# Optimization experiments

Hardware: AMD Instinct MI355X
Metric: run time of the kernel (lower is better)

The kernel has to match this reference:

```python
import jax, jax.numpy as jnp
import numpy as np

D = 1024
H = 16
HD = D // H
MLP = 4 * D
EPS = 1e-5


def layernorm(x, g, b):
    mu = jnp.mean(x, axis=-1, keepdims=True)
    var = jnp.mean(jnp.square(x - mu), axis=-1, keepdims=True)
    return (x - mu) * jax.lax.rsqrt(var + EPS) * g + b


def setup_inputs() -> dict:
    key = jax.random.key(0)
    ks = jax.random.split(key, 12)
    s = 0.02
    return {
        "x": jax.random.normal(ks[0], (2, 2048, D), jnp.float32),
        "ln1_g": jnp.ones((D,), jnp.float32),
        "ln1_b": jnp.zeros((D,), jnp.float32),
        "lnm_g": jnp.ones((D,), jnp.float32),
        "lnm_b": jnp.zeros((D,), jnp.float32),
        "qkv_w": jax.random.normal(ks[1], (D, 3 * D), jnp.float32) * s,
        "qkv_b": jnp.zeros((3 * D,), jnp.float32),
        "proj_w": jax.random.normal(ks[2], (D, D), jnp.float32) * s,
        "proj_b": jnp.zeros((D,), jnp.float32),
        "fc1_w": jax.random.normal(ks[3], (D, MLP), jnp.float32) * s,
        "fc1_b": jnp.zeros((MLP,), jnp.float32),
        "fc2_w": jax.random.normal(ks[4], (MLP, D), jnp.float32) * s,
        "fc2_b": jnp.zeros((D,), jnp.float32),
    }


def reference(x, ln1_g, ln1_b, lnm_g, lnm_b, qkv_w, qkv_b, proj_w, proj_b,
              fc1_w, fc1_b, fc2_w, fc2_b):
    B, N, _ = x.shape
    scale = HD ** -0.5
    # --- self-attention on norm1(x) ---
    h = layernorm(x, ln1_g, ln1_b)
    qkv = h @ qkv_w + qkv_b                       # [B, N, 3D]
    qkv = qkv.reshape(B, N, 3, H, HD)
    q, k, v = qkv[:, :, 0], qkv[:, :, 1], qkv[:, :, 2]  # [B, N, H, HD]
    attn = jnp.einsum("bqhd,bkhd->bhqk", q, k) * scale
    attn = jax.nn.softmax(attn, axis=-1)
    o = jnp.einsum("bhqk,bkhd->bqhd", attn, v).reshape(B, N, D)
    x = x + (o @ proj_w + proj_b)
    # --- MLP ---
    m = layernorm(x, lnm_g, lnm_b)
    m = jax.nn.gelu(m @ fc1_w + fc1_b, approximate=False)
    x = x + (m @ fc2_w + fc2_b)
    return x
```

## Files before the change

kernel.cpp:

```cpp
#include <hip/hip_runtime.h>

typedef __bf16 bf16_t;
typedef bf16_t bf16x8 __attribute__((ext_vector_type(8)));
typedef float f32x4 __attribute__((ext_vector_type(4)));
typedef unsigned short u16x8 __attribute__((ext_vector_type(8)));

#define MFMA(a, b, c) __builtin_amdgcn_mfma_f32_16x16x32_bf16(a, b, c, 0, 0, 0)

__device__ inline float exp2_fast(float x) {
  float r;
  asm volatile("v_exp_f32 %0, %1" : "=v"(r) : "v"(x));
  return r;
}

__device__ inline void gll16(const bf16_t* g, bf16_t* l) {
  __builtin_amdgcn_global_load_lds(
      (const __attribute__((address_space(1))) unsigned int*)(g),
      (__attribute__((address_space(3))) unsigned int*)(l), 16, 0, 0);
}

__device__ inline float gelu_f(float v) {
  float ax = fabsf(v) * 0.70710678118f;
  float t = __builtin_amdgcn_rcpf(1.0f + 0.3275911f * ax);
  float p = ((((1.061405429f * t - 1.453152027f) * t + 1.421413741f) * t -
              0.284496736f) * t + 0.254829592f) * t;
  float e = exp2_fast(-ax * ax * 1.4426950408889634f);
  float erf = 1.0f - p * e;
  erf = v < 0.f ? -erf : erf;
  return 0.5f * v * (1.0f + erf);
}

__global__ __launch_bounds__(256) void ln_kernel(const float* __restrict__ x,
                                                 const float* __restrict__ g,
                                                 const float* __restrict__ b,
                                                 bf16_t* __restrict__ out) {
  long row = blockIdx.x;
  const float4* xr = (const float4*)(x + row * 1024);
  float4 v = xr[threadIdx.x];
  float s = v.x + v.y + v.z + v.w;
  float s2 = v.x * v.x + v.y * v.y + v.z * v.z + v.w * v.w;
#pragma unroll
  for (int m = 32; m >= 1; m >>= 1) {
    s += __shfl_xor(s, m);
    s2 += __shfl_xor(s2, m);
  }
  __shared__ float red[8];
  int wid = threadIdx.x >> 6;
  if ((threadIdx.x & 63) == 0) {
    red[wid] = s;
    red[4 + wid] = s2;
  }
  __syncthreads();
  s = red[0] + red[1] + red[2] + red[3];
  s2 = red[4] + red[5] + red[6] + red[7];
  float mu = s * (1.f / 1024.f);
  float rs = rsqrtf(s2 * (1.f / 1024.f) - mu * mu + 1e-5f);
  float4 gv = ((const float4*)g)[threadIdx.x];
  float4 bv = ((const float4*)b)[threadIdx.x];
  bf16_t o0 = (bf16_t)((v.x - mu) * rs * gv.x + bv.x);
  bf16_t o1 = (bf16_t)((v.y - mu) * rs * gv.y + bv.y);
  bf16_t o2 = (bf16_t)((v.z - mu) * rs * gv.z + bv.z);
  bf16_t o3 = (bf16_t)((v.w - mu) * rs * gv.w + bv.w);
  ushort4 pk;
  pk.x = *(unsigned short*)&o0;
  pk.y = *(unsigned short*)&o1;
  pk.z = *(unsigned short*)&o2;
  pk.w = *(unsigned short*)&o3;
  *(ushort4*)(out + row * 1024 + threadIdx.x * 4) = pk;
}

__global__ void wconv_kernel(const float* __restrict__ W, bf16_t* __restrict__ Wt,
                             int K, int N) {
  __shared__ float t[32][33];
  int n0 = blockIdx.x * 32, k0 = blockIdx.y * 32;
#pragma unroll
  for (int s = 0; s < 4; s++) {
    int k = threadIdx.y + s * 8;
    t[k][threadIdx.x] = W[(long)(k0 + k) * N + n0 + threadIdx.x];
  }
  __syncthreads();
#pragma unroll
  for (int s = 0; s < 4; s++) {
    int n = threadIdx.y + s * 8;
    Wt[(long)(n0 + n) * K + k0 + threadIdx.x] = (bf16_t)t[threadIdx.x][n];
  }
}

#define STAGE_PTR(DA, DB, k0)                \
  gll16(ga + (k0), DA + w * 1024);           \
  gll16(ga + (k0) + rowstep, DA + w * 1024 + 512); \
  gll16(gb + (k0), DB + w * 1024);           \
  gll16(gb + (k0) + rowstep, DB + w * 1024 + 512);

#define COMPUTE(LA, LB)                                                \
  {                                                                    \
    bf16x8 af[4], bfr[4];                                              \
    _Pragma("unroll") for (int mt = 0; mt < 4; mt++) af[mt] =          \
        *(const bf16x8*)(LA + (wm + mt * 16 + l15) * 32 + quad * 8);   \
    _Pragma("unroll") for (int nt = 0; nt < 4; nt++) bfr[nt] =         \
        *(const bf16x8*)(LB + (wn + nt * 16 + l15) * 32 + quad * 8);   \
    _Pragma("unroll") for (int mt = 0; mt < 4; mt++)                   \
        _Pragma("unroll") for (int nt = 0; nt < 4; nt++) acc[mt][nt] = \
            MFMA(af[mt], bfr[nt], acc[mt][nt]);                        \
  }

#define WB4 asm volatile("s_waitcnt vmcnt(4)\ns_barrier" ::: "memory")
#define WB0 asm volatile("s_waitcnt vmcnt(0)\ns_barrier" ::: "memory")

__global__ __launch_bounds__(256) void gemm_kernel(
    const bf16_t* __restrict__ A, const bf16_t* __restrict__ Bt,
    const float* __restrict__ bias, const float* __restrict__ resid,
    void* __restrict__ Cout, int M, int N, int K, int epi) {
  __shared__ bf16_t lA0[128 * 32], lB0[128 * 32];
  __shared__ bf16_t lA1[128 * 32], lB1[128 * 32];
  __shared__ bf16_t lA2[128 * 32], lB2[128 * 32];
  int tid = threadIdx.x;
  int bn = blockIdx.x, bm = blockIdx.y;
  int kchunk = K / gridDim.z;
  int kbeg = blockIdx.z * kchunk, kend = kbeg + kchunk;

  int lane = tid & 63, w = tid >> 6;
  int quad = lane >> 4, l15 = lane & 15;
  int wm = (w & 1) * 64, wn = (w >> 1) * 64;

  f32x4 acc[4][4];
#pragma unroll
  for (int i = 0; i < 4; i++)
#pragma unroll
    for (int j = 0; j < 4; j++) acc[i][j] = (f32x4){0.f, 0.f, 0.f, 0.f};

  const bf16_t* ga = A + (long)(bm * 128 + w * 32 + (lane >> 2)) * K + (lane & 3) * 8;
  const bf16_t* gb = Bt + (long)(bn * 128 + w * 32 + (lane >> 2)) * K + (lane & 3) * 8;
  long rowstep = (long)16 * K;

  int nit = (kend - kbeg) >> 5;
  bf16_t *A0 = lA0, *A1 = lA1, *A2 = lA2;
  bf16_t *B0 = lB0, *B1 = lB1, *B2 = lB2;
  STAGE_PTR(A0, B0, kbeg);
  STAGE_PTR(A1, B1, kbeg + 32);
  for (int i = 0; i < nit; i++) {
    if (i + 1 < nit) { WB4; } else { WB0; }
    if (i + 2 < nit) {
      int ks = kbeg + (i + 2) * 32;
      STAGE_PTR(A2, B2, ks);
    }
    COMPUTE(A0, B0);
    bf16_t* t;
    t = A0; A0 = A1; A1 = A2; A2 = t;
    t = B0; B0 = B1; B1 = B2; B2 = t;
  }

#pragma unroll
  for (int mt = 0; mt < 4; mt++) {
#pragma unroll
    for (int r = 0; r < 4; r++) {
      long row = bm * 128 + wm + mt * 16 + quad * 4 + r;
#pragma unroll
      for (int nt = 0; nt < 4; nt++) {
        int col = bn * 128 + wn + nt * 16 + l15;
        long idx = row * N + col;
        if (epi == 3) {
          ((float*)Cout)[(long)blockIdx.z * M * N + idx] = acc[mt][nt][r];
        } else {
          float v = acc[mt][nt][r] + bias[col];
          if (epi == 1) {
            ((float*)Cout)[idx] = v + resid[idx];
          } else if (epi == 2) {
            ((bf16_t*)Cout)[idx] = (bf16_t)gelu_f(v);
          } else {
            ((bf16_t*)Cout)[idx] = (bf16_t)v;
          }
        }
      }
    }
  }
}

__global__ __launch_bounds__(256) void reduce2_kernel(const float* __restrict__ p0,
                                                      const float* __restrict__ p1,
                                                      const float* __restrict__ bias,
                                                      const float* __restrict__ resid,
                                                      float* __restrict__ out) {
  long i = (long)blockIdx.x * 256 + threadIdx.x;
  float4 a = ((const float4*)p0)[i];
  float4 c = ((const float4*)p1)[i];
  float4 r = ((const float4*)resid)[i];
  float4 bv = ((const float4*)bias)[i & 255];
  float4 o;
  o.x = a.x + c.x + r.x + bv.x;
  o.y = a.y + c.y + r.y + bv.y;
  o.z = a.z + c.z + r.z + bv.z;
  o.w = a.w + c.w + r.w + bv.w;
  ((float4*)out)[i] = o;
}

#define LDV 72

__global__ __launch_bounds__(256) void attn_kernel(const bf16_t* __restrict__ qkv,
                                                   bf16_t* __restrict__ o) {
  const int LD = 3072;
  int flat = blockIdx.x;
  int slot = flat >> 3;
  int bh = (flat & 7) * 4 + (slot >> 5);
  int qt = slot & 31;
  int h = bh & 15, b = bh >> 4;

  int tid = threadIdx.x, w = tid >> 6, lane = tid & 63;
  int quad = lane >> 4, l15 = lane & 15;
  int qrow = qt * 64 + w * 16;
  const bf16_t* base = qkv + (long)b * 2048 * LD + h * 64;
  const bf16_t* Qp = base;
  const bf16_t* Kp = base + 1024;
  const bf16_t* Vp = base + 2048;

  __shared__ bf16_t lK[64 * 64];
  __shared__ bf16_t lV[64 * LDV];
  __shared__ bf16_t lP[4][16 * LDV];
  bf16_t* myp = lP[w];

  const bf16_t* kg =
      Kp + (long)(w * 16 + (lane >> 3)) * LD + (((lane & 7) ^ (lane >> 3)) & 7) * 8;
  bf16_t* lkd = lK + w * 1024;
  int kk = tid & 31;
  int d0 = (tid >> 5) * 8;
  const bf16_t* vg = Vp + (long)(2 * kk) * LD + d0;
  unsigned int* lvw = (unsigned int*)lV;

  bf16x8 qf[2];
#pragma unroll
  for (int d = 0; d < 2; d++)
    qf[d] = *(const bf16x8*)(Qp + (long)(qrow + l15) * LD + d * 32 + quad * 8);

  f32x4 oacc[4];
#pragma unroll
  for (int t = 0; t < 4; t++) oacc[t] = (f32x4){0.f, 0.f, 0.f, 0.f};
  float li_p[4] = {0.f, 0.f, 0.f, 0.f};
  const float c2 = 0.18033688011112042f;

  int sw0 = (quad ^ l15) & 7;
  int sw1 = ((quad + 4) ^ l15) & 7;

  for (int kt = 0; kt < 2048; kt += 64) {
    long koff = (long)kt * LD;
    u16x8 va = *(const u16x8*)(vg + koff);
    u16x8 vb = *(const u16x8*)(vg + koff + LD);
    __syncthreads();
    gll16(kg + koff, lkd);
    gll16(kg + koff + 8 * (long)LD, lkd + 512);
#pragma unroll
    for (int j = 0; j < 8; j++)
      lvw[(d0 + j) * (LDV / 2) + kk] = (unsigned int)va[j] | ((unsigned int)vb[j] << 16);
    __syncthreads();

    f32x4 s[4];
#pragma unroll
    for (int st = 0; st < 4; st++) {
      const bf16_t* krow = lK + (st * 16 + l15) * 64;
      f32x4 z = (f32x4){0.f, 0.f, 0.f, 0.f};
      z = MFMA(qf[0], *(const bf16x8*)(krow + sw0 * 8), z);
      s[st] = MFMA(qf[1], *(const bf16x8*)(krow + sw1 * 8), z);
    }

#pragma unroll
    for (int st = 0; st < 4; st++)
#pragma unroll
      for (int r = 0; r < 4; r++) {
        float p = exp2_fast(s[st][r] * c2);
        s[st][r] = p;
        li_p[r] += p;
      }

#pragma unroll
    for (int r = 0; r < 4; r++)
#pragma unroll
      for (int st = 0; st < 4; st++)
        myp[(quad * 4 + r) * LDV + st * 16 + l15] = (bf16_t)s[st][r];
    asm volatile("s_waitcnt lgkmcnt(0)" ::: "memory");

    bf16x8 pa0 = *(const bf16x8*)(myp + l15 * LDV + quad * 8);
    bf16x8 pa1 = *(const bf16x8*)(myp + l15 * LDV + 32 + quad * 8);
#pragma unroll
    for (int t = 0; t < 4; t++) {
      const bf16_t* vr = lV + (t * 16 + l15) * LDV + quad * 8;
      oacc[t] = MFMA(pa0, *(const bf16x8*)(vr), oacc[t]);
      oacc[t] = MFMA(pa1, *(const bf16x8*)(vr + 32), oacc[t]);
    }
  }

  float li[4];
#pragma unroll
  for (int r = 0; r < 4; r++) {
    float s = li_p[r];
#pragma unroll
    for (int x = 8; x >= 1; x >>= 1) s += __shfl_xor(s, x);
    li[r] = s;
  }
#pragma unroll
  for (int t = 0; t < 4; t++)
#pragma unroll
    for (int r = 0; r < 4; r++) {
      long q = qrow + quad * 4 + r;
      o[((long)b * 2048 + q) * 1024 + h * 64 + t * 16 + l15] =
          (bf16_t)(oacc[t][r] / li[r]);
    }
}

extern "C" void kernel_launch(void* const* d_in, const int* in_sizes, int n_in,
                              void* d_out, int out_size, void* d_ws, size_t ws_size,
                              hipStream_t stream) {
  (void)in_sizes; (void)n_in; (void)out_size; (void)ws_size;
  const float* x = (const float*)d_in[0];
  const float* ln1_g = (const float*)d_in[1];
  const float* ln1_b = (const float*)d_in[2];
  const float* lnm_g = (const float*)d_in[3];
  const float* lnm_b = (const float*)d_in[4];
  const float* qkv_w = (const float*)d_in[5];
  const float* qkv_b = (const float*)d_in[6];
  const float* proj_w = (const float*)d_in[7];
  const float* proj_b = (const float*)d_in[8];
  const float* fc1_w = (const float*)d_in[9];
  const float* fc1_b = (const float*)d_in[10];
  const float* fc2_w = (const float*)d_in[11];
  const float* fc2_b = (const float*)d_in[12];
  float* out = (float*)d_out;

  const int M = 4096;
  const int D_ = 1024, MLP_ = 4096, QKV = 3072;

  char* ws = (char*)d_ws;
  bf16_t* h = (bf16_t*)(ws);
  bf16_t* qkvb = (bf16_t*)(ws + (8u << 20));
  bf16_t* ob = (bf16_t*)(ws + (32u << 20));
  float* x1 = (float*)(ws + (40u << 20));
  bf16_t* mb = (bf16_t*)(ws + (56u << 20));
  bf16_t* gb = (bf16_t*)(ws + (64u << 20));
  bf16_t* qkv_wt = (bf16_t*)(ws + (96u << 20));
  bf16_t* proj_wt = (bf16_t*)(ws + (102u << 20));
  bf16_t* fc1_wt = (bf16_t*)(ws + (104u << 20));
  bf16_t* fc2_wt = (bf16_t*)(ws + (112u << 20));
  float* p01 = (float*)(ws);

  dim3 tb(32, 8);
  wconv_kernel<<<dim3(QKV / 32, D_ / 32), tb, 0, stream>>>(qkv_w, qkv_wt, D_, QKV);
  wconv_kernel<<<dim3(D_ / 32, D_ / 32), tb, 0, stream>>>(proj_w, proj_wt, D_, D_);
  wconv_kernel<<<dim3(MLP_ / 32, D_ / 32), tb, 0, stream>>>(fc1_w, fc1_wt, D_, MLP_);
  wconv_kernel<<<dim3(D_ / 32, MLP_ / 32), tb, 0, stream>>>(fc2_w, fc2_wt, MLP_, D_);

  ln_kernel<<<M, 256, 0, stream>>>(x, ln1_g, ln1_b, h);
  gemm_kernel<<<dim3(QKV / 128, M / 128), 256, 0, stream>>>(h, qkv_wt, qkv_b, nullptr,
                                                            qkvb, M, QKV, D_, 0);
  attn_kernel<<<1024, 256, 0, stream>>>(qkvb, ob);
  gemm_kernel<<<dim3(D_ / 128, M / 128), 256, 0, stream>>>(ob, proj_wt, proj_b, x, x1,
                                                           M, D_, D_, 1);
  ln_kernel<<<M, 256, 0, stream>>>(x1, lnm_g, lnm_b, mb);
  gemm_kernel<<<dim3(MLP_ / 128, M / 128), 256, 0, stream>>>(mb, fc1_wt, fc1_b, nullptr,
                                                             gb, M, MLP_, D_, 2);
  gemm_kernel<<<dim3(D_ / 128, M / 128, 2), 256, 0, stream>>>(gb, fc2_wt, nullptr,
                                                              nullptr, p01, M, D_,
                                                              MLP_, 3);
  reduce2_kernel<<<4096, 256, 0, stream>>>(p01, p01 + (long)M * D_, fc2_b, x1, out);
}
```

Before: 445.1 us.

## Double-buffer attention K/V, split-K proj with fused reduce+LN, 4-way split fc2

The attention kernel now double-buffers K and V tiles in LDS and prefetches the next tile while computing the current one, replacing two full barriers with one waitcnt-plus-barrier pair. The proj GEMM becomes a 2-way split-K with bf16 partials, and a new kernel fuses the partial reduction, bias, residual and the MLP layernorm. The fc2 GEMM moves from 2-way to 4-way split-K, and all split-K partials are stored as bf16 instead of fp32 to cut traffic. Storing partial sums in bf16 loses precision, and the proj split-K adds an extra partial write and read pass.

```diff
diff --git a/kernel.cpp b/kernel.cpp
--- a/kernel.cpp
+++ b/kernel.cpp
@@ -1,6 +1,7 @@
 #include <hip/hip_runtime.h>
 
 typedef __bf16 bf16_t;
+typedef bf16_t bf16x4 __attribute__((ext_vector_type(4)));
 typedef bf16_t bf16x8 __attribute__((ext_vector_type(8)));
 typedef float f32x4 __attribute__((ext_vector_type(4)));
 typedef unsigned short u16x8 __attribute__((ext_vector_type(8)));
@@ -160,7 +161,7 @@
         int col = bn * 128 + wn + nt * 16 + l15;
         long idx = row * N + col;
         if (epi == 3) {
-          ((float*)Cout)[(long)blockIdx.z * M * N + idx] = acc[mt][nt][r];
+          ((bf16_t*)Cout)[(long)blockIdx.z * M * N + idx] = (bf16_t)acc[mt][nt][r];
         } else {
           float v = acc[mt][nt][r] + bias[col];
           if (epi == 1) {
@@ -176,21 +177,72 @@
   }
 }
 
-__global__ __launch_bounds__(256) void reduce2_kernel(const float* __restrict__ p0,
-                                                      const float* __restrict__ p1,
+__global__ __launch_bounds__(256) void reduce_ln_kernel(
+    const bf16_t* __restrict__ p0, const bf16_t* __restrict__ p1,
+    const float* __restrict__ bias, const float* __restrict__ resid,
+    float* __restrict__ x1, const float* __restrict__ g,
+    const float* __restrict__ bb, bf16_t* __restrict__ mb) {
+  long row = blockIdx.x;
+  int t = threadIdx.x;
+  bf16x4 a = *(const bf16x4*)(p0 + row * 1024 + t * 4);
+  bf16x4 c = *(const bf16x4*)(p1 + row * 1024 + t * 4);
+  float4 r = ((const float4*)(resid + row * 1024))[t];
+  float4 bv = ((const float4*)bias)[t];
+  float4 v;
+  v.x = (float)a[0] + (float)c[0] + r.x + bv.x;
+  v.y = (float)a[1] + (float)c[1] + r.y + bv.y;
+  v.z = (float)a[2] + (float)c[2] + r.z + bv.z;
+  v.w = (float)a[3] + (float)c[3] + r.w + bv.w;
+  ((float4*)(x1 + row * 1024))[t] = v;
+  float s = v.x + v.y + v.z + v.w;
+  float s2 = v.x * v.x + v.y * v.y + v.z * v.z + v.w * v.w;
+#pragma unroll
+  for (int m = 32; m >= 1; m >>= 1) {
+    s += __shfl_xor(s, m);
+    s2 += __shfl_xor(s2, m);
+  }
+  __shared__ float red[8];
+  int wid = t >> 6;
+  if ((t & 63) == 0) {
+    red[wid] = s;
+    red[4 + wid] = s2;
+  }
+  __syncthreads();
+  s = red[0] + red[1] + red[2] + red[3];
+  s2 = red[4] + red[5] + red[6] + red[7];
+  float mu = s * (1.f / 1024.f);
+  float rs = rsqrtf(s2 * (1.f / 1024.f) - mu * mu + 1e-5f);
+  float4 gv = ((const float4*)g)[t];
+  float4 b2 = ((const float4*)bb)[t];
+  bf16_t o0 = (bf16_t)((v.x - mu) * rs * gv.x + b2.x);
+  bf16_t o1 = (bf16_t)((v.y - mu) * rs * gv.y + b2.y);
+  bf16_t o2 = (bf16_t)((v.z - mu) * rs * gv.z + b2.z);
+  bf16_t o3 = (bf16_t)((v.w - mu) * rs * gv.w + b2.w);
+  ushort4 pk;
+  pk.x = *(unsigned short*)&o0;
+  pk.y = *(unsigned short*)&o1;
+  pk.z = *(unsigned short*)&o2;
+  pk.w = *(unsigned short*)&o3;
+  *(ushort4*)(mb + row * 1024 + t * 4) = pk;
+}
+
+__global__ __launch_bounds__(256) void reduce4_kernel(const bf16_t* __restrict__ p,
                                                       const float* __restrict__ bias,
                                                       const float* __restrict__ resid,
                                                       float* __restrict__ out) {
   long i = (long)blockIdx.x * 256 + threadIdx.x;
-  float4 a = ((const float4*)p0)[i];
-  float4 c = ((const float4*)p1)[i];
+  const long MN = (long)4096 * 1024;
+  bf16x4 a0 = *(const bf16x4*)(p + i * 4);
+  bf16x4 a1 = *(const bf16x4*)(p + MN + i * 4);
+  bf16x4 a2 = *(const bf16x4*)(p + 2 * MN + i * 4);
+  bf16x4 a3 = *(const bf16x4*)(p + 3 * MN + i * 4);
   float4 r = ((const float4*)resid)[i];
   float4 bv = ((const float4*)bias)[i & 255];
   float4 o;
-  o.x = a.x + c.x + r.x + bv.x;
-  o.y = a.y + c.y + r.y + bv.y;
-  o.z = a.z + c.z + r.z + bv.z;
-  o.w = a.w + c.w + r.w + bv.w;
+  o.x = (float)a0[0] + (float)a1[0] + (float)a2[0] + (float)a3[0] + r.x + bv.x;
+  o.y = (float)a0[1] + (float)a1[1] + (float)a2[1] + (float)a3[1] + r.y + bv.y;
+  o.z = (float)a0[2] + (float)a1[2] + (float)a2[2] + (float)a3[2] + r.z + bv.z;
+  o.w = (float)a0[3] + (float)a1[3] + (float)a2[3] + (float)a3[3] + r.w + bv.w;
   ((float4*)out)[i] = o;
 }
 
@@ -213,19 +265,21 @@
   const bf16_t* Kp = base + 1024;
   const bf16_t* Vp = base + 2048;
 
-  __shared__ bf16_t lK[64 * 64];
-  __shared__ bf16_t lV[64 * LDV];
+  __shared__ bf16_t lK[2][64 * 64];
+  __shared__ bf16_t lV[2][64 * LDV];
   __shared__ bf16_t lP[4][16 * LDV];
   bf16_t* myp = lP[w];
 
   const bf16_t* kg =
       Kp + (long)(w * 16 + (lane >> 3)) * LD + (((lane & 7) ^ (lane >> 3)) & 7) * 8;
-  bf16_t* lkd = lK + w * 1024;
   int kk = tid & 31;
   int d0 = (tid >> 5) * 8;
   const bf16_t* vg = Vp + (long)(2 * kk) * LD + d0;
-  unsigned int* lvw = (unsigned int*)lV;
-
+
+  gll16(kg, lK[0] + w * 1024);
+  gll16(kg + 8 * (long)LD, lK[0] + w * 1024 + 512);
+  u16x8 va = *(const u16x8*)(vg);
+  u16x8 vb = *(const u16x8*)(vg + LD);
   bf16x8 qf[2];
 #pragma unroll
   for (int d = 0; d < 2; d++)
@@ -240,22 +294,27 @@
   int sw0 = (quad ^ l15) & 7;
   int sw1 = ((quad + 4) ^ l15) & 7;
 
-  for (int kt = 0; kt < 2048; kt += 64) {
-    long koff = (long)kt * LD;
-    u16x8 va = *(const u16x8*)(vg + koff);
-    u16x8 vb = *(const u16x8*)(vg + koff + LD);
-    __syncthreads();
-    gll16(kg + koff, lkd);
-    gll16(kg + koff + 8 * (long)LD, lkd + 512);
+  for (int it = 0; it < 32; it++) {
+    int cur = it & 1, nxt = cur ^ 1;
+    asm volatile("s_waitcnt vmcnt(0)\ns_barrier" ::: "memory");
+    unsigned int* lvw = (unsigned int*)lV[cur];
 #pragma unroll
     for (int j = 0; j < 8; j++)
       lvw[(d0 + j) * (LDV / 2) + kk] = (unsigned int)va[j] | ((unsigned int)vb[j] << 16);
-    __syncthreads();
+    u16x8 va_n = va, vb_n = vb;
+    if (it + 1 < 32) {
+      long koff2 = (long)(it + 1) * 64 * LD;
+      gll16(kg + koff2, lK[nxt] + w * 1024);
+      gll16(kg + koff2 + 8 * (long)LD, lK[nxt] + w * 1024 + 512);
+      va_n = *(const u16x8*)(vg + koff2);
+      vb_n = *(const u16x8*)(vg + koff2 + LD);
+    }
+    asm volatile("s_waitcnt lgkmcnt(0)\ns_barrier" ::: "memory");
 
     f32x4 s[4];
 #pragma unroll
     for (int st = 0; st < 4; st++) {
-      const bf16_t* krow = lK + (st * 16 + l15) * 64;
+      const bf16_t* krow = lK[cur] + (st * 16 + l15) * 64;
       f32x4 z = (f32x4){0.f, 0.f, 0.f, 0.f};
       z = MFMA(qf[0], *(const bf16x8*)(krow + sw0 * 8), z);
       s[st] = MFMA(qf[1], *(const bf16x8*)(krow + sw1 * 8), z);
@@ -281,10 +340,12 @@
     bf16x8 pa1 = *(const bf16x8*)(myp + l15 * LDV + 32 + quad * 8);
 #pragma unroll
     for (int t = 0; t < 4; t++) {
-      const bf16_t* vr = lV + (t * 16 + l15) * LDV + quad * 8;
+      const bf16_t* vr = lV[cur] + (t * 16 + l15) * LDV + quad * 8;
       oacc[t] = MFMA(pa0, *(const bf16x8*)(vr), oacc[t]);
       oacc[t] = MFMA(pa1, *(const bf16x8*)(vr + 32), oacc[t]);
     }
+    va = va_n;
+    vb = vb_n;
   }
 
   float li[4];
@@ -338,7 +399,8 @@
   bf16_t* proj_wt = (bf16_t*)(ws + (102u << 20));
   bf16_t* fc1_wt = (bf16_t*)(ws + (104u << 20));
   bf16_t* fc2_wt = (bf16_t*)(ws + (112u << 20));
-  float* p01 = (float*)(ws);
+  bf16_t* p_proj = (bf16_t*)(ws + (8u << 20));
+  bf16_t* p_fc2 = (bf16_t*)(ws);
 
   dim3 tb(32, 8);
   wconv_kernel<<<dim3(QKV / 32, D_ / 32), tb, 0, stream>>>(qkv_w, qkv_wt, D_, QKV);
@@ -350,13 +412,15 @@
   gemm_kernel<<<dim3(QKV / 128, M / 128), 256, 0, stream>>>(h, qkv_wt, qkv_b, nullptr,
                                                             qkvb, M, QKV, D_, 0);
   attn_kernel<<<1024, 256, 0, stream>>>(qkvb, ob);
-  gemm_kernel<<<dim3(D_ / 128, M / 128), 256, 0, stream>>>(ob, proj_wt, proj_b, x, x1,
-                                                           M, D_, D_, 1);
-  ln_kernel<<<M, 256, 0, stream>>>(x1, lnm_g, lnm_b, mb);
+  gemm_kernel<<<dim3(D_ / 128, M / 128, 2), 256, 0, stream>>>(ob, proj_wt, nullptr,
+                                                              nullptr, p_proj, M, D_,
+                                                              D_, 3);
+  reduce_ln_kernel<<<M, 256, 0, stream>>>(p_proj, p_proj + (long)M * D_, proj_b, x,
+                                          x1, lnm_g, lnm_b, mb);
   gemm_kernel<<<dim3(MLP_ / 128, M / 128), 256, 0, stream>>>(mb, fc1_wt, fc1_b, nullptr,
                                                              gb, M, MLP_, D_, 2);
-  gemm_kernel<<<dim3(D_ / 128, M / 128, 2), 256, 0, stream>>>(gb, fc2_wt, nullptr,
-                                                              nullptr, p01, M, D_,
+  gemm_kernel<<<dim3(D_ / 128, M / 128, 4), 256, 0, stream>>>(gb, fc2_wt, nullptr,
+                                                              nullptr, p_fc2, M, D_,
                                                               MLP_, 3);
-  reduce2_kernel<<<4096, 256, 0, stream>>>(p01, p01 + (long)M * D_, fc2_b, x1, out);
-}
+  reduce4_kernel<<<4096, 256, 0, stream>>>(p_fc2, fc2_b, x1, out);
+}
```

New measurement: 454.8 us. 1.02x slower.
